# Kernel optimization log

Measured on AMD Instinct MI355X. Metric: run time of the kernel, lower is better.

Reference implementation:

```python
import jax, jax.numpy as jnp
import numpy as np

D = 256          # object_dim == query_dim
HG = 1024        # g hidden / output width
HF0, HF1 = 1024, 512
OUT_F = 256
N = 32768        # number of objects


def _mlp_g(h, W0, b0, W1, b1, W2, b2):
    # g=True: ReLU after every layer, including output.
    h = jax.nn.relu(h @ W0 + b0)
    h = jax.nn.relu(h @ W1 + b1)
    return jax.nn.relu(h @ W2 + b2)


def _mlp_f(h, W0, b0, W1, b1, W2, b2):
    # f: ReLU on hidden layers, linear output.
    h = jax.nn.relu(h @ W0 + b0)
    h = jax.nn.relu(h @ W1 + b1)
    return h @ W2 + b2


def setup_inputs() -> dict:
    key = jax.random.key(0)
    ks = jax.random.split(key, 16)
    def lin(k, fan_in, fan_out):
        s = 1.0 / np.sqrt(fan_in)
        kw, kb = jax.random.split(k)
        W = jax.random.uniform(kw, (fan_in, fan_out), jnp.float32, -s, s)
        b = jax.random.uniform(kb, (fan_out,), jnp.float32, -s, s)
        return W, b
    x = jax.random.normal(ks[0], (N, D), jnp.float32)
    q = jax.random.normal(ks[1], (D,), jnp.float32)
    g_W0, g_b0 = lin(ks[2], 3 * D, HG)
    g_W1, g_b1 = lin(ks[3], HG, HG)
    g_W2, g_b2 = lin(ks[4], HG, HG)
    f_W0, f_b0 = lin(ks[5], HG, HF0)
    f_W1, f_b1 = lin(ks[6], HF0, HF1)
    f_W2, f_b2 = lin(ks[7], HF1, OUT_F)
    return dict(x=x, q=q,
                g_W0=g_W0, g_b0=g_b0, g_W1=g_W1, g_b1=g_b1, g_W2=g_W2, g_b2=g_b2,
                f_W0=f_W0, f_b0=f_b0, f_W1=f_W1, f_b1=f_b1, f_W2=f_W2, f_b2=f_b2)


def reference(x, q, g_W0, g_b0, g_W1, g_b1, g_W2, g_b2,
              f_W0, f_b0, f_W1, f_b1, f_W2, f_b2):
    n = x.shape[0]
    # mode 4: adjacent pairs (o_i, o_{i+1}), query concatenated to each pair.
    pair_concat = jnp.concatenate(
        [x[:-1], x[1:], jnp.broadcast_to(q, (n - 1, q.shape[0]))], axis=-1)  # (n-1, 3D)
    relations = _mlp_g(pair_concat, g_W0, g_b0, g_W1, g_b1, g_W2, g_b2)       # (n-1, HG)
    embedding = jnp.sum(relations, axis=0)                                     # (HG,)
    return _mlp_f(embedding, f_W0, f_b0, f_W1, f_b1, f_W2, f_b2)               # (OUT_F,)
```

## Files before the change

### kernel.cpp

```cpp
#include <hip/hip_runtime.h>

typedef __attribute__((ext_vector_type(8))) short short8;
typedef __attribute__((ext_vector_type(4))) float floatx4;
typedef __attribute__((ext_vector_type(4))) unsigned int uint32x4;

#define NROWS 32768L
#define NVALID 32767L
#define HGDIM 1024

__device__ __forceinline__ unsigned short f2bf_rne(float f) {
    union { float f; unsigned u; } v; v.f = f;
    unsigned r = v.u + 0x7fffu + ((v.u >> 16) & 1u);
    return (unsigned short)(r >> 16);
}

__device__ __forceinline__ void gload_lds16(const void* g, void* l) {
    __builtin_amdgcn_global_load_lds(
        (const __attribute__((address_space(1))) void*)g,
        (__attribute__((address_space(3))) void*)l,
        16, 0, 0);
}

__global__ void cvt_x(const float* __restrict__ x, unsigned short* __restrict__ xb,
                      long nx, long ntot4) {
    long i = (long)blockIdx.x * 256 + threadIdx.x;
    if (i >= ntot4) return;
    long i4 = i * 4;
    float4 v = make_float4(0.f, 0.f, 0.f, 0.f);
    if (i4 < nx) v = *(const float4*)(x + i4);
    ushort4 o;
    o.x = f2bf_rne(v.x); o.y = f2bf_rne(v.y); o.z = f2bf_rne(v.z); o.w = f2bf_rne(v.w);
    *(ushort4*)(xb + i4) = o;
}

__global__ void transpose_cvt(const float* __restrict__ W, unsigned short* __restrict__ Wt,
                              int K, int N) {
    __shared__ float tile[32][33];
    int tx = threadIdx.x & 31, ty = threadIdx.x >> 5;
    int nb = blockIdx.x * 32, kb = blockIdx.y * 32;
    #pragma unroll
    for (int i = 0; i < 32; i += 8)
        tile[ty + i][tx] = W[(size_t)(kb + ty + i) * N + (nb + tx)];
    __syncthreads();
    #pragma unroll
    for (int i = 0; i < 32; i += 8)
        Wt[(size_t)(nb + ty + i) * K + (kb + tx)] = f2bf_rne(tile[tx][ty + i]);
}

template<bool RELU_IN>
__global__ void fc_partial(const float* __restrict__ in, const float* __restrict__ W,
                           const float* __restrict__ bias, float* __restrict__ out,
                           int N) {
    __shared__ float s_in[128];
    int j = blockIdx.x * 256 + threadIdx.x;
    int k0 = blockIdx.y * 128;
    if (threadIdx.x < 128) {
        float v = in[k0 + threadIdx.x];
        if (RELU_IN) v = fmaxf(v, 0.f);
        s_in[threadIdx.x] = v;
    }
    __syncthreads();
    float acc = (blockIdx.y == 0) ? bias[j] : 0.f;
    #pragma unroll 4
    for (int k = 0; k < 128; ++k)
        acc += s_in[k] * W[(size_t)(k0 + k) * N + j];
    atomicAdd(&out[j], acc);
}


#define SBAR() __builtin_amdgcn_sched_barrier(0)

#define P_PRE(N) do { SBAR(); __builtin_amdgcn_s_barrier(); \
    asm volatile("s_waitcnt lgkmcnt(" #N ")" ::: "memory"); SBAR(); \
    __builtin_amdgcn_s_setprio(1); } while (0)

#define P_POSTW(N) do { __builtin_amdgcn_s_setprio(0); SBAR(); \
    asm volatile("s_waitcnt vmcnt(" #N ")" ::: "memory"); SBAR(); \
    __builtin_amdgcn_s_barrier(); SBAR(); } while (0)

#define STAGE(buf, region, T) do { \
    if ((region) >= 2) { \
        const unsigned short* _g = gA + (long)(((region) & 1) * 128) * lda + (long)(T) * 64; \
        char* _d = (char*)&lds[buf][0][((region) & 1) * 128][0] + t * 16; \
        gload_lds16(_g, _d); \
        gload_lds16(_g + 64L * lda, _d + 8192); \
    } else { \
        const unsigned short* _g = gB + (long)(((region) & 1) * 128) * ldb + (long)(T) * 64; \
        char* _d = (char*)&lds[buf][1][((region) & 1) * 128][0] + t * 16; \
        gload_lds16(_g, _d); \
        gload_lds16(_g + 64L * ldb, _d + 8192); \
    } } while (0)

#define LDA4(dst, buf, mbase, ks) do { _Pragma("unroll") for (int _q = 0; _q < 4; ++_q) \
    dst[_q] = *(const short8*)((const char*)&lds[buf][0][arowb + ((mbase) + _q) * 16][0] + ((ks) ? cb1 : cb0)); } while (0)

#define LDB4(dst, buf, ks) do { _Pragma("unroll") for (int _q = 0; _q < 4; ++_q) \
    dst[_q] = *(const short8*)((const char*)&lds[buf][1][browb + _q * 16][0] + ((ks) ? cb1 : cb0)); } while (0)

#define MFMA16(AF, BF, MO) do { _Pragma("unroll") for (int _mf = 0; _mf < 4; ++_mf) { \
    _Pragma("unroll") for (int _nf = 0; _nf < 4; ++_nf) \
        acc[(MO) + _mf][_nf] = __builtin_amdgcn_mfma_f32_16x16x32_bf16(AF[_mf], BF[_nf], acc[(MO) + _mf][_nf], 0, 0, 0); } } while (0)

template<int COLSUM>
__global__ __launch_bounds__(512, 2)
void gemm256(const unsigned short* __restrict__ A, int lda,
             const unsigned short* __restrict__ Bt, int ldb,
             const float* __restrict__ bias, int K,
             unsigned short* __restrict__ Hout,
             float* __restrict__ emb, long row0g, long nvalid,
             int mblocks) {
    __shared__ alignas(16) unsigned short lds[2][2][256][64];

    const int t = threadIdx.x;
    int nwg = gridDim.x, bid = blockIdx.x, swz;
    if ((nwg & 7) == 0) { int cpx = nwg >> 3; swz = (bid & 7) * cpx + (bid >> 3); }
    else swz = bid;
    const int mb = swz >> 2, nb = swz & 3;
    const long m0 = (long)mb * 256;
    const int n0 = nb * 256;

    const int srow = t >> 3;
    const int ssc = (t & 7) ^ (srow & 7);
    const unsigned short* gA = A + (m0 + srow) * (long)lda + ssc * 8;
    const unsigned short* gB = Bt + ((long)n0 + srow) * (long)ldb + ssc * 8;

    const int lane = t & 63;
    const int wv = t >> 6;
    const int wm = wv >> 2, wn = wv & 3;
    const int arowb = wm * 128 + (lane & 15);
    const int browb = wn * 64 + (lane & 15);
    const int c0x = (lane >> 4) ^ (lane & 7);
    const int cb0 = c0x * 16;
    const int cb1 = (c0x ^ 4) * 16;

    floatx4 acc[8][4] = {};

    const int NT = K >> 6;
    const int NI = NT >> 1;

    short8 bE0[4], bE1[4], bO0[4], bO1[4];
    short8 aE0[4], aE1[4], aE2[4], aE3[4], aO0[4], aO1[4], aO2[4], aO3[4];

    STAGE(0, 0, 0); STAGE(0, 1, 0); STAGE(0, 2, 0); STAGE(0, 3, 0);
    STAGE(1, 0, 1); STAGE(1, 1, 1);
    asm volatile("s_waitcnt vmcnt(4)" ::: "memory");
    SBAR();
    __builtin_amdgcn_s_barrier();
    SBAR();
    LDB4(bE0, 0, 0); LDA4(aE0, 0, 0, 0);

    for (int i = 0; i < NI; ++i) {
        const int O = 2 * i + 1;
        int N2 = 2 * i + 2; if (N2 >= NT) N2 = 0;
        int P2 = 2 * i + 3; if (P2 >= NT) P2 = 1;

        LDA4(aE1, 0, 4, 0);
        STAGE(1, 2, O);
        P_PRE(4); MFMA16(aE0, bE0, 0); P_POSTW(4);
        LDB4(bE1, 0, 1); LDA4(aE2, 0, 0, 1);
        STAGE(1, 3, O);
        P_PRE(8); MFMA16(aE1, bE0, 4); P_POSTW(4);
        LDA4(aE3, 0, 4, 1);
        STAGE(0, 0, N2);
        P_PRE(4); MFMA16(aE2, bE1, 0); P_POSTW(4);
        LDB4(bO0, 1, 0); LDA4(aO0, 1, 0, 0);
        STAGE(0, 1, N2);
        P_PRE(8); MFMA16(aE3, bE1, 4); P_POSTW(4);
        LDA4(aO1, 1, 4, 0);
        STAGE(0, 2, N2);
        P_PRE(4); MFMA16(aO0, bO0, 0); P_POSTW(4);
        LDB4(bO1, 1, 1); LDA4(aO2, 1, 0, 1);
        STAGE(0, 3, N2);
        P_PRE(8); MFMA16(aO1, bO0, 4); P_POSTW(4);
        LDA4(aO3, 1, 4, 1);
        STAGE(1, 0, P2);
        P_PRE(4); MFMA16(aO2, bO1, 0); P_POSTW(2);
        LDB4(bE0, 0, 0); LDA4(aE0, 0, 0, 0);
        STAGE(1, 1, P2);
        P_PRE(8); MFMA16(aO3, bO1, 4); P_POSTW(4);
    }
    asm volatile("s_waitcnt vmcnt(0) lgkmcnt(0)" ::: "memory");
    SBAR();
    __builtin_amdgcn_s_barrier();

    if (COLSUM == 0) {
        char* slb = (char*)&lds[0][0][0][0];
        #pragma unroll
        for (int nf = 0; nf < 4; ++nf) {
            int ncol = wn * 64 + nf * 16 + (lane & 15);
            float bv = bias[n0 + ncol];
            #pragma unroll
            for (int mf = 0; mf < 8; ++mf) {
                int rbase = wm * 128 + mf * 16 + ((lane >> 4) << 2);
                #pragma unroll
                for (int j = 0; j < 4; ++j) {
                    int row = rbase + j;
                    float v = fmaxf(acc[mf][nf][j] + bv, 0.f);
                    int byte = row * 512 + ((ncol * 2) ^ ((row & 7) << 4));
                    *(unsigned short*)(slb + byte) = f2bf_rne(v);
                }
            }
        }
        __syncthreads();
        {
            int rsub = t >> 5;
            int cb = (t & 31) * 16;
            #pragma unroll
            for (int i2 = 0; i2 < 16; ++i2) {
                int row = i2 * 16 + rsub;
                const char* src = slb + row * 512 + (cb ^ ((row & 7) << 4));
                uint32x4 v = *(const uint32x4*)src;
                char* dst = (char*)Hout + ((size_t)(m0 + row) * HGDIM + n0) * 2 + cb;
                *(uint32x4*)dst = v;
            }
        }
    } else {
        #pragma unroll
        for (int nf = 0; nf < 4; ++nf) {
            int ncol = n0 + wn * 64 + nf * 16 + (lane & 15);
            float bv = bias[ncol];
            float cs = 0.f;
            #pragma unroll
            for (int mf = 0; mf < 8; ++mf) {
                long rbase = row0g + m0 + wm * 128 + mf * 16 + ((lane >> 4) << 2);
                #pragma unroll
                for (int j = 0; j < 4; ++j) {
                    float v = fmaxf(acc[mf][nf][j] + bv, 0.f);
                    if (rbase + j < nvalid) cs += v;
                }
            }
            cs += __shfl_xor(cs, 16);
            cs += __shfl_xor(cs, 32);
            if ((lane >> 4) == 0) atomicAdd(&emb[ncol], cs);
        }
    }
}

extern "C" void kernel_launch(void* const* d_in, const int* in_sizes, int n_in,
                              void* d_out, int out_size, void* d_ws, size_t ws_size,
                              hipStream_t stream) {
    const float* x   = (const float*)d_in[0];
    const float* q   = (const float*)d_in[1];
    const float* gW0 = (const float*)d_in[2];
    const float* gb0 = (const float*)d_in[3];
    const float* gW1 = (const float*)d_in[4];
    const float* gb1 = (const float*)d_in[5];
    const float* gW2 = (const float*)d_in[6];
    const float* gb2 = (const float*)d_in[7];
    const float* fW0 = (const float*)d_in[8];
    const float* fb0 = (const float*)d_in[9];
    const float* fW1 = (const float*)d_in[10];
    const float* fb1 = (const float*)d_in[11];
    const float* fW2 = (const float*)d_in[12];
    const float* fb2 = (const float*)d_in[13];
    float* out = (float*)d_out;

    char* ws = (char*)d_ws;
    size_t off = 0;
    auto alloc = [&](size_t bytes) -> char* {
        char* p = ws + off;
        off += (bytes + 255) & ~(size_t)255;
        return p;
    };
    unsigned short* xb  = (unsigned short*)alloc((NROWS + 1) * 256 * 2);
    unsigned short* w0t = (unsigned short*)alloc((size_t)1024 * 512 * 2);
    unsigned short* w1t = (unsigned short*)alloc((size_t)1024 * 1024 * 2);
    unsigned short* w2t = (unsigned short*)alloc((size_t)1024 * 1024 * 2);
    float* c0  = (float*)alloc(4096);
    float* emb = (float*)alloc(4096);
    float* e1  = (float*)alloc(4096);
    float* e2  = (float*)alloc(4096);
    size_t fixed = off;
    size_t avail = (ws_size > fixed) ? ws_size - fixed : 0;
    long CR = (long)((avail / 2) / (HGDIM * 2));
    CR = (CR / 512) * 512;
    if (CR > NROWS) CR = NROWS;
    if (CR < 512) CR = 512;
    unsigned short* H0 = (unsigned short*)alloc((size_t)CR * HGDIM * 2);
    unsigned short* H1 = (unsigned short*)alloc((size_t)CR * HGDIM * 2);

    hipMemsetAsync(c0, 0, 4 * 4096, stream);
    hipMemsetAsync(out, 0, 256 * sizeof(float), stream);

    long ntot4 = (NROWS + 1) * 256 / 4;
    cvt_x<<<dim3((unsigned)((ntot4 + 255) / 256)), 256, 0, stream>>>(x, xb, NROWS * 256, ntot4);

    transpose_cvt<<<dim3(32, 16), 256, 0, stream>>>(gW0, w0t, 512, 1024);
    transpose_cvt<<<dim3(32, 32), 256, 0, stream>>>(gW1, w1t, 1024, 1024);
    transpose_cvt<<<dim3(32, 32), 256, 0, stream>>>(gW2, w2t, 1024, 1024);

    fc_partial<false><<<dim3(4, 2), 256, 0, stream>>>(q, gW0 + (size_t)512 * 1024, gb0, c0, 1024);

    for (long r0 = 0; r0 < NROWS; r0 += CR) {
        long rows = NROWS - r0; if (rows > CR) rows = CR;
        int mblocks = (int)(rows / 256);
        dim3 g((unsigned)(mblocks * 4));
        gemm256<0><<<g, 512, 0, stream>>>(xb + r0 * 256, 256, w0t, 512, c0, 512,
                                          H0, nullptr, 0, 0, mblocks);
        gemm256<0><<<g, 512, 0, stream>>>(H0, 1024, w1t, 1024, gb1, 1024,
                                          H1, nullptr, 0, 0, mblocks);
        gemm256<1><<<g, 512, 0, stream>>>(H1, 1024, w2t, 1024, gb2, 1024,
                                          nullptr, emb, r0, NVALID, mblocks);
    }

    fc_partial<false><<<dim3(4, 8), 256, 0, stream>>>(emb, fW0, fb0, e1, 1024);
    fc_partial<true><<<dim3(2, 8), 256, 0, stream>>>(e1, fW1, fb1, e2, 512);
    fc_partial<true><<<dim3(1, 4), 256, 0, stream>>>(e2, fW2, fb2, out, 256);
}
```

Baseline: 241.1 us.

## Store hidden activations in MFMA fragment layout and load A directly to registers

Layer outputs H0/H1 are now written in a pre-tiled MFMA A-fragment layout, so the layer-2 and layer-3 GEMMs read A operands straight from global memory into registers instead of staging them through LDS. Only B tiles go through LDS, now with a 4-deep buffer, and the warp tiling changes to 4x8 fragments per wave. The aim is to cut LDS traffic and staging barriers for the large K=1024 GEMMs. The cost is higher register pressure and exposure to global-load latency on the A path, and the workspace size calculation now reserves a pad.

```diff
diff --git a/kernel.cpp b/kernel.cpp
--- a/kernel.cpp
+++ b/kernel.cpp
@@ -67,17 +67,14 @@
     atomicAdd(&out[j], acc);
 }
 
-
 #define SBAR() __builtin_amdgcn_sched_barrier(0)
 
 #define P_PRE(N) do { SBAR(); __builtin_amdgcn_s_barrier(); \
     asm volatile("s_waitcnt lgkmcnt(" #N ")" ::: "memory"); SBAR(); \
     __builtin_amdgcn_s_setprio(1); } while (0)
-
 #define P_POSTW(N) do { __builtin_amdgcn_s_setprio(0); SBAR(); \
     asm volatile("s_waitcnt vmcnt(" #N ")" ::: "memory"); SBAR(); \
     __builtin_amdgcn_s_barrier(); SBAR(); } while (0)
-
 #define STAGE(buf, region, T) do { \
     if ((region) >= 2) { \
         const unsigned short* _g = gA + (long)(((region) & 1) * 128) * lda + (long)(T) * 64; \
@@ -90,24 +87,19 @@
         gload_lds16(_g, _d); \
         gload_lds16(_g + 64L * ldb, _d + 8192); \
     } } while (0)
-
 #define LDA4(dst, buf, mbase, ks) do { _Pragma("unroll") for (int _q = 0; _q < 4; ++_q) \
     dst[_q] = *(const short8*)((const char*)&lds[buf][0][arowb + ((mbase) + _q) * 16][0] + ((ks) ? cb1 : cb0)); } while (0)
-
 #define LDB4(dst, buf, ks) do { _Pragma("unroll") for (int _q = 0; _q < 4; ++_q) \
     dst[_q] = *(const short8*)((const char*)&lds[buf][1][browb + _q * 16][0] + ((ks) ? cb1 : cb0)); } while (0)
-
 #define MFMA16(AF, BF, MO) do { _Pragma("unroll") for (int _mf = 0; _mf < 4; ++_mf) { \
     _Pragma("unroll") for (int _nf = 0; _nf < 4; ++_nf) \
         acc[(MO) + _mf][_nf] = __builtin_amdgcn_mfma_f32_16x16x32_bf16(AF[_mf], BF[_nf], acc[(MO) + _mf][_nf], 0, 0, 0); } } while (0)
 
-template<int COLSUM>
 __global__ __launch_bounds__(512, 2)
-void gemm256(const unsigned short* __restrict__ A, int lda,
+void gemm_l1(const unsigned short* __restrict__ A, int lda,
              const unsigned short* __restrict__ Bt, int ldb,
              const float* __restrict__ bias, int K,
              unsigned short* __restrict__ Hout,
-             float* __restrict__ emb, long row0g, long nvalid,
              int mblocks) {
     __shared__ alignas(16) unsigned short lds[2][2][256][64];
 
@@ -134,7 +126,6 @@
     const int cb1 = (c0x ^ 4) * 16;
 
     floatx4 acc[8][4] = {};
-
     const int NT = K >> 6;
     const int NI = NT >> 1;
 
@@ -183,50 +174,192 @@
     SBAR();
     __builtin_amdgcn_s_barrier();
 
+    char* slb = (char*)&lds[0][0][0][0];
+    #pragma unroll
+    for (int nf = 0; nf < 4; ++nf) {
+        int col = wn * 64 + nf * 16 + (lane & 15);
+        float bv = bias[n0 + col];
+        #pragma unroll
+        for (int mf = 0; mf < 8; ++mf) {
+            int rbase = wm * 128 + mf * 16 + ((lane >> 4) << 2);
+            #pragma unroll
+            for (int j = 0; j < 4; ++j) {
+                int row = rbase + j;
+                float v = fmaxf(acc[mf][nf][j] + bv, 0.f);
+                int byte = row * 512 + ((col * 2) ^ ((row & 7) << 4));
+                *(unsigned short*)(slb + byte) = f2bf_rne(v);
+            }
+        }
+    }
+    __syncthreads();
+    {
+        int xr = (lane & 7) << 4;
+        #pragma unroll
+        for (int s = 0; s < 2; ++s) {
+            int mt = wv * 2 + s;
+            const char* srcrow = slb + (mt * 16 + (lane & 15)) * 512;
+            #pragma unroll
+            for (int kt = 0; kt < 8; ++kt) {
+                uint32x4 v = *(const uint32x4*)(srcrow + ((kt * 64 + ((lane >> 4) << 4)) ^ xr));
+                unsigned short* dst = Hout + (((size_t)(mb * 16 + mt) * 32) + (nb * 8 + kt)) * 512 + lane * 8;
+                *(uint32x4*)dst = v;
+            }
+        }
+    }
+}
+
+
+#define A_LD(dst, ks, C) do { _Pragma("unroll") for (int _m = 0; _m < 4; ++_m) \
+    dst[_m][ks] = *(const short8*)(aPtr[_m] + aoff + (C)); } while (0)
+
+#define B_RD(dst, buf, ks) do { _Pragma("unroll") for (int _n = 0; _n < 8; ++_n) \
+    dst[_n] = *(const short8*)((const char*)&lds[buf][browb + _n * 16][0] + ((ks) ? cb1 : cb0)); } while (0)
+
+#define B_STG(buf, half, T) do { \
+    const unsigned short* _g = gB + (long)((half) * 128) * ldb + (long)(T) * 64; \
+    char* _d = (char*)&lds[buf][(half) * 128][0] + t * 16; \
+    gload_lds16(_g, _d); \
+    gload_lds16(_g + 64L * ldb, _d + 8192); } while (0)
+
+#define MFMA32(AF, ks, BF) do { _Pragma("unroll") for (int _m = 0; _m < 4; ++_m) { \
+    _Pragma("unroll") for (int _n = 0; _n < 8; ++_n) \
+        acc[_m][_n] = __builtin_amdgcn_mfma_f32_16x16x32_bf16(AF[_m][ks], BF[_n], acc[_m][_n], 0, 0, 0); } } while (0)
+
+#define Q_PRE() do { SBAR(); \
+    asm volatile("s_waitcnt vmcnt(12)" ::: "memory"); SBAR(); \
+    __builtin_amdgcn_s_barrier(); \
+    asm volatile("s_waitcnt lgkmcnt(8)" ::: "memory"); SBAR(); \
+    __builtin_amdgcn_s_setprio(1); } while (0)
+#define Q_POST() do { __builtin_amdgcn_s_setprio(0); SBAR(); } while (0)
+
+template<int COLSUM>
+__global__ __launch_bounds__(512, 2)
+void gemm_areg(const unsigned short* __restrict__ Afrag,
+               const unsigned short* __restrict__ Bt, int ldb,
+               const float* __restrict__ bias, int K,
+               unsigned short* __restrict__ Hout,
+               float* __restrict__ emb, long row0g, long nvalid,
+               int mblocks) {
+    __shared__ alignas(16) unsigned short lds[4][256][64];
+
+    const int t = threadIdx.x;
+    int nwg = gridDim.x, bid = blockIdx.x, swz;
+    if ((nwg & 7) == 0) { int cpx = nwg >> 3; swz = (bid & 7) * cpx + (bid >> 3); }
+    else swz = bid;
+    const int mb = swz >> 2, nb = swz & 3;
+    const long m0 = (long)mb * 256;
+    const int n0 = nb * 256;
+
+    const int lane = t & 63;
+    const int wv = t >> 6;
+    const int wm = wv >> 1, wn = wv & 1;
+    const int browb = wn * 128 + (lane & 15);
+    const int c0x = (lane >> 4) ^ (lane & 7);
+    const int cb0 = c0x * 16;
+    const int cb1 = (c0x ^ 4) * 16;
+
+    const int srow = t >> 3;
+    const int ssc = (t & 7) ^ (srow & 7);
+    const unsigned short* gB = Bt + ((long)n0 + srow) * (long)ldb + ssc * 8;
+
+    const int KT = K >> 5;
+    const int NT = K >> 6;
+    const int NI = NT >> 2;
+
+    const int mtb = mb * 16 + wm * 4;
+    const char* aPtr[4];
+    #pragma unroll
+    for (int mf = 0; mf < 4; ++mf)
+        aPtr[mf] = (const char*)Afrag + ((size_t)(mtb + mf) * KT) * 1024 + lane * 16;
+
+    floatx4 acc[4][8] = {};
+    short8 aP[4][2], aQ[4][2], bX[8], bY[8];
+    size_t aoff = 0;
+
+    B_STG(0, 0, 0); B_STG(0, 1, 0); B_STG(1, 0, 1); B_STG(1, 1, 1); B_STG(2, 0, 2);
+    A_LD(aP, 0, 0); A_LD(aP, 1, 1024);
+    asm volatile("s_waitcnt vmcnt(4)" ::: "memory");
+    SBAR();
+    __builtin_amdgcn_s_barrier();
+    SBAR();
+    B_RD(bX, 0, 0);
+
+    for (int j = 0; j < NI; ++j) {
+        int Ta = 4 * j + 2;
+        int Tb = 4 * j + 3;
+        int Tc = 4 * j + 4; if (Tc >= NT) Tc -= NT;
+        int Td = 4 * j + 5; if (Td >= NT) Td -= NT;
+        int Te = 4 * j + 6; if (Te >= NT) Te -= NT;
+
+        A_LD(aQ, 0, 2048); B_RD(bY, 0, 1); B_STG(2, 1, Ta);
+        Q_PRE(); MFMA32(aP, 0, bX); Q_POST();
+        A_LD(aQ, 1, 3072); B_RD(bX, 1, 0); B_STG(3, 0, Tb);
+        Q_PRE(); MFMA32(aP, 1, bY); Q_POST();
+        A_LD(aP, 0, 4096); B_RD(bY, 1, 1); B_STG(3, 1, Tb);
+        Q_PRE(); MFMA32(aQ, 0, bX); Q_POST();
+        A_LD(aP, 1, 5120); B_RD(bX, 2, 0); B_STG(0, 0, Tc);
+        Q_PRE(); MFMA32(aQ, 1, bY); Q_POST();
+        A_LD(aQ, 0, 6144); B_RD(bY, 2, 1); B_STG(0, 1, Tc);
+        Q_PRE(); MFMA32(aP, 0, bX); Q_POST();
+        A_LD(aQ, 1, 7168); B_RD(bX, 3, 0); B_STG(1, 0, Td);
+        Q_PRE(); MFMA32(aP, 1, bY); Q_POST();
+        A_LD(aP, 0, 8192); B_RD(bY, 3, 1); B_STG(1, 1, Td);
+        Q_PRE(); MFMA32(aQ, 0, bX); Q_POST();
+        A_LD(aP, 1, 9216); B_RD(bX, 0, 0); B_STG(2, 0, Te);
+        Q_PRE(); MFMA32(aQ, 1, bY); Q_POST();
+
+        aoff += 8192;
+    }
+    asm volatile("s_waitcnt vmcnt(0) lgkmcnt(0)" ::: "memory");
+    SBAR();
+    __builtin_amdgcn_s_barrier();
+
     if (COLSUM == 0) {
-        char* slb = (char*)&lds[0][0][0][0];
+        char* slb = (char*)&lds[0][0][0];
         #pragma unroll
-        for (int nf = 0; nf < 4; ++nf) {
-            int ncol = wn * 64 + nf * 16 + (lane & 15);
-            float bv = bias[n0 + ncol];
+        for (int nf = 0; nf < 8; ++nf) {
+            int col = wn * 128 + nf * 16 + (lane & 15);
+            float bv = bias[n0 + col];
             #pragma unroll
-            for (int mf = 0; mf < 8; ++mf) {
-                int rbase = wm * 128 + mf * 16 + ((lane >> 4) << 2);
+            for (int mf = 0; mf < 4; ++mf) {
+                int rbase = wm * 64 + mf * 16 + ((lane >> 4) << 2);
                 #pragma unroll
-                for (int j = 0; j < 4; ++j) {
-                    int row = rbase + j;
-                    float v = fmaxf(acc[mf][nf][j] + bv, 0.f);
-                    int byte = row * 512 + ((ncol * 2) ^ ((row & 7) << 4));
+                for (int j2 = 0; j2 < 4; ++j2) {
+                    int row = rbase + j2;
+                    float v = fmaxf(acc[mf][nf][j2] + bv, 0.f);
+                    int byte = row * 512 + ((col * 2) ^ ((row & 7) << 4));
                     *(unsigned short*)(slb + byte) = f2bf_rne(v);
                 }
             }
         }
         __syncthreads();
         {
-            int rsub = t >> 5;
-            int cb = (t & 31) * 16;
+            int xr = (lane & 7) << 4;
             #pragma unroll
-            for (int i2 = 0; i2 < 16; ++i2) {
-                int row = i2 * 16 + rsub;
-                const char* src = slb + row * 512 + (cb ^ ((row & 7) << 4));
-                uint32x4 v = *(const uint32x4*)src;
-                char* dst = (char*)Hout + ((size_t)(m0 + row) * HGDIM + n0) * 2 + cb;
-                *(uint32x4*)dst = v;
+            for (int s = 0; s < 2; ++s) {
+                int mt = wv * 2 + s;
+                const char* srcrow = slb + (mt * 16 + (lane & 15)) * 512;
+                #pragma unroll
+                for (int kt = 0; kt < 8; ++kt) {
+                    uint32x4 v = *(const uint32x4*)(srcrow + ((kt * 64 + ((lane >> 4) << 4)) ^ xr));
+                    unsigned short* dst = Hout + (((size_t)(mb * 16 + mt) * 32) + (nb * 8 + kt)) * 512 + lane * 8;
+                    *(uint32x4*)dst = v;
+                }
             }
         }
     } else {
         #pragma unroll
-        for (int nf = 0; nf < 4; ++nf) {
-            int ncol = n0 + wn * 64 + nf * 16 + (lane & 15);
+        for (int nf = 0; nf < 8; ++nf) {
+            int ncol = n0 + wn * 128 + nf * 16 + (lane & 15);
             float bv = bias[ncol];
             float cs = 0.f;
             #pragma unroll
-            for (int mf = 0; mf < 8; ++mf) {
-                long rbase = row0g + m0 + wm * 128 + mf * 16 + ((lane >> 4) << 2);
+            for (int mf = 0; mf < 4; ++mf) {
+                long rbase = row0g + m0 + wm * 64 + mf * 16 + ((lane >> 4) << 2);
                 #pragma unroll
-                for (int j = 0; j < 4; ++j) {
-                    float v = fmaxf(acc[mf][nf][j] + bv, 0.f);
-                    if (rbase + j < nvalid) cs += v;
+                for (int j2 = 0; j2 < 4; ++j2) {
+                    float v = fmaxf(acc[mf][nf][j2] + bv, 0.f);
+                    if (rbase + j2 < nvalid) cs += v;
                 }
             }
             cs += __shfl_xor(cs, 16);
@@ -271,7 +404,8 @@
     float* e1  = (float*)alloc(4096);
     float* e2  = (float*)alloc(4096);
     size_t fixed = off;
-    size_t avail = (ws_size > fixed) ? ws_size - fixed : 0;
+    size_t pad = 262144;
+    size_t avail = (ws_size > fixed + pad) ? ws_size - fixed - pad : 0;
     long CR = (long)((avail / 2) / (HGDIM * 2));
     CR = (CR / 512) * 512;
     if (CR > NROWS) CR = NROWS;
@@ -295,12 +429,12 @@
         long rows = NROWS - r0; if (rows > CR) rows = CR;
         int mblocks = (int)(rows / 256);
         dim3 g((unsigned)(mblocks * 4));
-        gemm256<0><<<g, 512, 0, stream>>>(xb + r0 * 256, 256, w0t, 512, c0, 512,
-                                          H0, nullptr, 0, 0, mblocks);
-        gemm256<0><<<g, 512, 0, stream>>>(H0, 1024, w1t, 1024, gb1, 1024,
-                                          H1, nullptr, 0, 0, mblocks);
-        gemm256<1><<<g, 512, 0, stream>>>(H1, 1024, w2t, 1024, gb2, 1024,
-                                          nullptr, emb, r0, NVALID, mblocks);
+        gemm_l1<<<g, 512, 0, stream>>>(xb + r0 * 256, 256, w0t, 512, c0, 512,
+                                       H0, mblocks);
+        gemm_areg<0><<<g, 512, 0, stream>>>(H0, w1t, 1024, gb1, 1024,
+                                            H1, nullptr, 0, 0, mblocks);
+        gemm_areg<1><<<g, 512, 0, stream>>>(H1, w2t, 1024, gb2, 1024,
+                                            nullptr, emb, r0, NVALID, mblocks);
     }
 
     fc_partial<false><<<dim3(4, 8), 256, 0, stream>>>(emb, fW0, fb0, e1, 1024);
```

Result: slower. 430.5 us (+78.5%).
